# Optimization experiments

Hardware: AMD Instinct MI355X
Metric: run time of the kernel (lower is better)

Reference implementation:

```python
import jax, jax.numpy as jnp
import numpy as np

B, L1, L2 = 16, 32, 128
DEC = 512       # decoder_size
MEM = 512       # memory_bank_size
TOP = 50        # topic_num


def setup_inputs() -> dict:
    key = jax.random.key(0)
    ks = jax.random.split(key, 16)
    s = lambda fan_in: 1.0 / np.sqrt(fan_in)
    inp = {
        "decoder_state": jax.random.normal(ks[0], (B, DEC), jnp.float32),
        "doc_memory": jax.random.normal(ks[1], (B, L1, MEM), jnp.float32),
        "word_memory": jax.random.normal(ks[2], (B, L1, L2, MEM), jnp.float32),
        "topic_dist": jax.random.uniform(ks[3], (B, TOP), jnp.float32),
        "doc_mask": jnp.ones((B, L1), jnp.int32),
        "word_mask": jnp.ones((B, L1, L2), jnp.int32),
        # HierAttention params (PyTorch Linear weight layout: [out, in])
        "Wv": jax.random.uniform(ks[4], (1, DEC), jnp.float32, -s(DEC), s(DEC)),
        "Wd": jax.random.uniform(ks[5], (DEC, DEC), jnp.float32, -s(DEC), s(DEC)),
        "Wt": jax.random.uniform(ks[6], (DEC, TOP), jnp.float32, -s(TOP), s(TOP)),
        "Wm": jax.random.uniform(ks[7], (DEC, MEM), jnp.float32, -s(MEM), s(MEM)),
        # doc_attention (inner Attention) params
        "Wv2": jax.random.uniform(ks[8], (1, DEC), jnp.float32, -s(DEC), s(DEC)),
        "Wd2": jax.random.uniform(ks[9], (DEC, DEC), jnp.float32, -s(DEC), s(DEC)),
        "Wt2": jax.random.uniform(ks[10], (DEC, TOP), jnp.float32, -s(TOP), s(TOP)),
        "Wm2": jax.random.uniform(ks[11], (DEC, MEM), jnp.float32, -s(MEM), s(MEM)),
    }
    return inp


def reference(decoder_state, doc_memory, word_memory, topic_dist,
              doc_mask, word_mask,
              Wv, Wd, Wt, Wm, Wv2, Wd2, Wt2, Wm2):
    neg_inf = jnp.float32(-jnp.inf)

    # ---- word-level (HierAttention.score) ----
    enc_feat = jnp.einsum('bqwm,dm->bqwd', word_memory, Wm)      # [B,L1,L2,DEC]
    dec_feat = decoder_state @ Wd.T                              # [B,DEC]
    top_feat = topic_dist @ Wt.T                                 # [B,DEC]
    e = jnp.tanh(enc_feat + (dec_feat + top_feat)[:, None, None, :])
    word_scores = jnp.einsum('bqwd,od->bqw', e, Wv)[..., 0] if Wv.shape[0] != 1 else jnp.einsum('bqwd,d->bqw', e, Wv[0])
    word_scores = jnp.where(word_mask == 0, neg_inf, word_scores)
    word_attn = jax.nn.softmax(word_scores, axis=-1)             # [B,L1,L2]

    # ---- doc-level (Attention.score) ----
    enc_feat_d = jnp.einsum('bqm,dm->bqd', doc_memory, Wm2)      # [B,L1,DEC]
    dec_feat_d = decoder_state @ Wd2.T                           # [B,DEC]
    top_feat_d = topic_dist @ Wt2.T                              # [B,DEC]
    e_d = jnp.tanh(enc_feat_d + (dec_feat_d + top_feat_d)[:, None, :])
    doc_scores = jnp.einsum('bqd,d->bq', e_d, Wv2[0])            # [B,L1]
    doc_scores = jnp.where(doc_mask == 0, neg_inf, doc_scores)
    doc_attn = jax.nn.softmax(doc_scores, axis=-1)               # [B,L1]

    # ---- combine ----
    rescaled = doc_attn[..., None] * word_attn                   # [B,L1,L2]
    context = jnp.einsum('bqw,bqwm->bm', rescaled, word_memory)  # [B,MEM]
    return context, rescaled
```

## Files before the change

### kernel.cpp

```cpp
#include <hip/hip_runtime.h>
#include <hip/hip_bf16.h>
#include <math.h>

#define BATCH 16
#define L1 32
#define L2 128
#define DEC 512
#define MEM 512
#define TOPN 50
#define NROWS (BATCH * L1 * L2)
#define NBQ (BATCH * L1)

typedef short short8 __attribute__((ext_vector_type(8)));
typedef float f32x16 __attribute__((ext_vector_type(16)));

#define WS_WP     0
#define WS_WP2    131072
#define WS_BIAS1  262144
#define WS_BIAS2  270336
#define WS_DOCSC  278528

__device__ __forceinline__ unsigned int pkbf(float a, float b) {
    __hip_bfloat162 h = __float22bfloat162_rn(float2{a, b});
    union { __hip_bfloat162 h; unsigned int u; } c{h};
    return c.u;
}

__device__ __forceinline__ float fast_tanh(float x) {
    return 1.f - 2.f / (__expf(2.f * x) + 1.f);
}

__global__ __launch_bounds__(256) void setup_kernel(
    const float* __restrict__ Wm, const float* __restrict__ Wm2,
    unsigned short* __restrict__ Wp, unsigned short* __restrict__ Wp2,
    const float* __restrict__ dec, const float* __restrict__ topic,
    const float* __restrict__ Wd, const float* __restrict__ Wt,
    const float* __restrict__ Wd2, const float* __restrict__ Wt2,
    float* __restrict__ bias1, float* __restrict__ bias2,
    float* __restrict__ ctx_out)
{
    const int bid = blockIdx.x;
    const int tid = threadIdx.x;
    if (bid < 128) {
        int s = bid * 256 + tid;
        int C = s >> 10;
        int u = s & 1023;
        int nt = u >> 6, k8 = (u >> 5) & 1, n_in = u & 31;
        int d = nt * 32 + n_in;
        int k = C * 16 + k8 * 8;

        const float4* src = (const float4*)(Wm + (size_t)d * DEC + k);
        float4 v0 = src[0], v1 = src[1];
        uint4 v;
        v.x = pkbf(v0.x, v0.y); v.y = pkbf(v0.z, v0.w);
        v.z = pkbf(v1.x, v1.y); v.w = pkbf(v1.z, v1.w);
        ((uint4*)Wp)[s] = v;

        const float4* src2 = (const float4*)(Wm2 + (size_t)d * DEC + k);
        float4 w0 = src2[0], w1 = src2[1];
        uint4 w;
        w.x = pkbf(w0.x, w0.y); w.y = pkbf(w0.z, w0.w);
        w.z = pkbf(w1.x, w1.y); w.w = pkbf(w1.z, w1.w);
        ((uint4*)Wp2)[s] = w;
    } else if (bid < 128 + 4096) {
        int gw = (bid - 128) * 4 + (tid >> 6);
        int lane = tid & 63;
        int mat = gw >> 13;
        int rem = gw & 8191;
        int bb = rem >> 9;
        int d = rem & 511;

        const float* wrow = (mat ? Wd2 : Wd) + (size_t)d * DEC;
        const float* drow = dec + (size_t)bb * DEC;
        float4 a0 = ((const float4*)wrow)[lane * 2];
        float4 a1 = ((const float4*)wrow)[lane * 2 + 1];
        float4 x0 = ((const float4*)drow)[lane * 2];
        float4 x1 = ((const float4*)drow)[lane * 2 + 1];
        float acc = a0.x * x0.x;
        acc = fmaf(a0.y, x0.y, acc);
        acc = fmaf(a0.z, x0.z, acc);
        acc = fmaf(a0.w, x0.w, acc);
        acc = fmaf(a1.x, x1.x, acc);
        acc = fmaf(a1.y, x1.y, acc);
        acc = fmaf(a1.z, x1.z, acc);
        acc = fmaf(a1.w, x1.w, acc);
        const float* trow = (mat ? Wt2 : Wt) + (size_t)d * TOPN;
        if (lane < TOPN) acc = fmaf(trow[lane], topic[bb * TOPN + lane], acc);
#pragma unroll
        for (int o = 1; o <= 32; o <<= 1) acc += __shfl_xor(acc, o);
        if (lane == 0) (mat ? bias2 : bias1)[bb * DEC + d] = acc;
    } else {
        int i = (bid - (128 + 4096)) * 256 + tid;
        float4 z = {0.f, 0.f, 0.f, 0.f};
        ((float4*)ctx_out)[i * 2] = z;
        ((float4*)ctx_out)[i * 2 + 1] = z;
    }
}

__global__ __launch_bounds__(256, 2) void score_all_kernel(
    const float* __restrict__ Xw,
    const float* __restrict__ Xd,
    const unsigned short* __restrict__ Wp,
    const unsigned short* __restrict__ Wp2,
    const float* __restrict__ Wv, const float* __restrict__ Wv2,
    const float* __restrict__ bias1, const float* __restrict__ bias2,
    float* __restrict__ word_scores,
    float* __restrict__ doc_scores)
{
    __shared__ __align__(16) char lsA[64 * 1040];
    __shared__ float red[4][64];

    const int bid = blockIdx.x;
    const int tid = threadIdx.x;
    const bool isdoc = (bid >= 1024);

    const float* X;
    const unsigned short* Wpp;
    const float* Wvp;
    const float* bias;
    float* outp;
    int r0, bshift;
    if (isdoc) { X = Xd; Wpp = Wp2; Wvp = Wv2; bias = bias2; outp = doc_scores; r0 = (bid - 1024) * 64; bshift = 5; }
    else       { X = Xw; Wpp = Wp;  Wvp = Wv;  bias = bias1; outp = word_scores; r0 = bid * 64; bshift = 12; }

    {
        const int kf4 = tid & 127;
        const int rb0 = tid >> 7;
        const float4* Xs = (const float4*)X + (size_t)r0 * 128 + kf4;
        float4 va[8], vb[8];
#pragma unroll
        for (int i = 0; i < 8; ++i) va[i] = Xs[(size_t)(2 * i + rb0) * 128];
#pragma unroll
        for (int blk = 0; blk < 4; ++blk) {
            float4* cur = (blk & 1) ? vb : va;
            float4* nxt = (blk & 1) ? va : vb;
            if (blk < 3) {
#pragma unroll
                for (int i = 0; i < 8; ++i)
                    nxt[i] = Xs[(size_t)(2 * (8 * (blk + 1) + i) + rb0) * 128];
            }
#pragma unroll
            for (int i = 0; i < 8; ++i) {
                int row = 2 * (8 * blk + i) + rb0;
                uint2 w;
                w.x = pkbf(cur[i].x, cur[i].y);
                w.y = pkbf(cur[i].z, cur[i].w);
                *(uint2*)(lsA + (size_t)row * 1040 + kf4 * 8) = w;
            }
        }
    }
    __syncthreads();

    const int lane = tid & 63;
    const int wid = tid >> 6;
    const int col = lane & 31;
    const int h = lane >> 5;

    const char* aB0 = lsA + (size_t)col * 1040 + h * 16;
    const char* aB1 = aB0 + 32 * 1040;

    const uint4* Bq = (const uint4*)Wpp;
    const int bBase = wid * 128 + lane;
#define BOFF(s) ((size_t)((s) & 31) * 1024 + (size_t)((s) >> 5) * 512 + bBase)
#define MFMA(a, bb, c) __builtin_amdgcn_mfma_f32_32x32x16_bf16(a, bb, c, 0, 0, 0)

    uint4 rbf[8][2];
#pragma unroll
    for (int i = 0; i < 8; ++i) { rbf[i][0] = Bq[BOFF(i)]; rbf[i][1] = Bq[BOFF(i) + 64]; }

    float preg0 = 0.f, preg1 = 0.f;
    const int b0i = (r0) >> bshift;
    const int b1i = (r0 + 32) >> bshift;

#pragma unroll
    for (int P = 0; P < 2; ++P) {
        f32x16 acc0, acc1, acc2, acc3;
        acc0 = acc1 = acc2 = acc3 =
            (f32x16){0.f,0.f,0.f,0.f, 0.f,0.f,0.f,0.f, 0.f,0.f,0.f,0.f, 0.f,0.f,0.f,0.f};
#pragma unroll
        for (int t = 0; t < 32; ++t) {
            const int s = P * 32 + t;
            short8 a0 = *(const short8*)(aB0 + t * 32);
            short8 a1 = *(const short8*)(aB1 + t * 32);
            union { uint4 u; short8 s8; } c0{rbf[s & 7][0]}, c1{rbf[s & 7][1]};
            if (s < 56) { rbf[s & 7][0] = Bq[BOFF(s + 8)]; rbf[s & 7][1] = Bq[BOFF(s + 8) + 64]; }
            acc0 = MFMA(a0, c0.s8, acc0);
            acc1 = MFMA(a0, c1.s8, acc1);
            acc2 = MFMA(a1, c0.s8, acc2);
            acc3 = MFMA(a1, c1.s8, acc3);
        }
        const int d0 = P * 256 + wid * 64 + col;
        const float wv0 = Wvp[d0], wv1 = Wvp[d0 + 32];
        {
            const float bs0 = bias[b0i * DEC + d0], bs1 = bias[b0i * DEC + d0 + 32];
#pragma unroll
            for (int r = 0; r < 16; ++r) {
                float val = fmaf(wv0, fast_tanh(acc0[r] + bs0),
                                 wv1 * fast_tanh(acc1[r] + bs1));
                val += __shfl_xor(val, 16);
                val += __shfl_xor(val, 8);
                val += __shfl_xor(val, 4);
                val += __shfl_xor(val, 2);
                val += __shfl_xor(val, 1);
                preg0 += (col == r) ? val : 0.f;
            }
        }
        {
            const float bs0 = bias[b1i * DEC + d0], bs1 = bias[b1i * DEC + d0 + 32];
#pragma unroll
            for (int r = 0; r < 16; ++r) {
                float val = fmaf(wv0, fast_tanh(acc2[r] + bs0),
                                 wv1 * fast_tanh(acc3[r] + bs1));
                val += __shfl_xor(val, 16);
                val += __shfl_xor(val, 8);
                val += __shfl_xor(val, 4);
                val += __shfl_xor(val, 2);
                val += __shfl_xor(val, 1);
                preg1 += (col == r) ? val : 0.f;
            }
        }
    }

    const int rowin = (col & 3) + 8 * (col >> 2) + 4 * h;
    if (col < 16) {
        red[wid][rowin] = preg0;
        red[wid][32 + rowin] = preg1;
    }
    __syncthreads();
    if (tid < 64)
        outp[r0 + tid] = red[0][tid] + red[1][tid] + red[2][tid] + red[3][tid];
}

__global__ __launch_bounds__(256, 4) void combine_kernel(
    const float* __restrict__ X,
    const float* __restrict__ doc_scores,
    const int* __restrict__ doc_mask,
    const int* __restrict__ word_mask,
    float* __restrict__ rescaled_out,
    float* __restrict__ ctx_out)
{
    __shared__ float sS[128];
    __shared__ float rmax2[2], rsum2[2];
    __shared__ float s_dattn;
    __shared__ __align__(16) float4 part[128];

    const int tid = threadIdx.x;
    const int lane = tid & 63;
    const int wid = tid >> 6;
    const int bq = blockIdx.x;
    const int r0 = bq * L2;
    const int b = bq >> 5;
    const int q = bq & 31;

    if (tid < 32) {
        int di = b * 32 + tid;
        float dsv = doc_scores[di];
        if (doc_mask[di] == 0) dsv = -INFINITY;
        float mx = dsv;
#pragma unroll
        for (int o = 1; o <= 16; o <<= 1) mx = fmaxf(mx, __shfl_xor(mx, o));
        float e = __expf(dsv - mx);
        float sum = e;
#pragma unroll
        for (int o = 1; o <= 16; o <<= 1) sum += __shfl_xor(sum, o);
        if (tid == q) s_dattn = e / sum;
    }

    float e = 0.f, sv = 0.f;
    if (tid < 128) {
        sv = rescaled_out[r0 + tid];
        if (word_mask[r0 + tid] == 0) sv = -INFINITY;
        float mx = sv;
#pragma unroll
        for (int o = 1; o <= 32; o <<= 1) mx = fmaxf(mx, __shfl_xor(mx, o));
        if (lane == 0) rmax2[wid] = mx;
    }
    __syncthreads();
    if (tid < 128) {
        float mx = fmaxf(rmax2[0], rmax2[1]);
        e = __expf(sv - mx);
        float sum = e;
#pragma unroll
        for (int o = 1; o <= 32; o <<= 1) sum += __shfl_xor(sum, o);
        if (lane == 0) rsum2[wid] = sum;
    }
    __syncthreads();
    if (tid < 128) {
        float sum = rsum2[0] + rsum2[1];
        float resc = s_dattn * (e / sum);
        sS[tid] = resc;
        rescaled_out[r0 + tid] = resc;
    }
    __syncthreads();

    const int hh = tid >> 7;
    const int m4 = tid & 127;
    const float4* Xr = (const float4*)X + (size_t)(r0 + hh * 64) * 128 + m4;
    float4 a = {0.f, 0.f, 0.f, 0.f};
#pragma unroll 8
    for (int i = 0; i < 64; ++i) {
        float rr = sS[hh * 64 + i];
        float4 v = Xr[(size_t)i * 128];
        a.x = fmaf(rr, v.x, a.x);
        a.y = fmaf(rr, v.y, a.y);
        a.z = fmaf(rr, v.z, a.z);
        a.w = fmaf(rr, v.w, a.w);
    }
    if (hh) part[m4] = a;
    __syncthreads();
    if (hh == 0) {
        float4 p0 = part[m4];
        a.x += p0.x; a.y += p0.y; a.z += p0.z; a.w += p0.w;
        float* dst = ctx_out + (size_t)b * MEM + m4 * 4;
        atomicAdd(dst + 0, a.x);
        atomicAdd(dst + 1, a.y);
        atomicAdd(dst + 2, a.z);
        atomicAdd(dst + 3, a.w);
    }
}

extern "C" void kernel_launch(void* const* d_in, const int* in_sizes, int n_in,
                              void* d_out, int out_size, void* d_ws, size_t ws_size,
                              hipStream_t stream) {
    const float* decoder_state = (const float*)d_in[0];
    const float* doc_memory    = (const float*)d_in[1];
    const float* word_memory   = (const float*)d_in[2];
    const float* topic_dist    = (const float*)d_in[3];
    const int*   doc_mask      = (const int*)d_in[4];
    const int*   word_mask     = (const int*)d_in[5];
    const float* Wv  = (const float*)d_in[6];
    const float* Wd  = (const float*)d_in[7];
    const float* Wt  = (const float*)d_in[8];
    const float* Wm  = (const float*)d_in[9];
    const float* Wv2 = (const float*)d_in[10];
    const float* Wd2 = (const float*)d_in[11];
    const float* Wt2 = (const float*)d_in[12];
    const float* Wm2 = (const float*)d_in[13];

    float* ws = (float*)d_ws;
    unsigned short* Wp  = (unsigned short*)(ws + WS_WP);
    unsigned short* Wp2 = (unsigned short*)(ws + WS_WP2);
    float* bias1       = ws + WS_BIAS1;
    float* bias2       = ws + WS_BIAS2;
    float* doc_scores  = ws + WS_DOCSC;

    float* ctx_out      = (float*)d_out;
    float* rescaled_out = (float*)d_out + BATCH * MEM;

    setup_kernel<<<128 + 4096 + 4, 256, 0, stream>>>(Wm, Wm2, Wp, Wp2,
                                                     decoder_state, topic_dist,
                                                     Wd, Wt, Wd2, Wt2, bias1, bias2, ctx_out);
    score_all_kernel<<<1024 + 8, 256, 0, stream>>>(word_memory, doc_memory, Wp, Wp2,
                                                   Wv, Wv2, bias1, bias2,
                                                   rescaled_out, doc_scores);
    combine_kernel<<<NBQ, 256, 0, stream>>>(word_memory, doc_scores, doc_mask, word_mask,
                                            rescaled_out, ctx_out);
}
```

Measured before the change: 342.0 us.

## Fuse word scoring with softmax and context reduction into one kernel

Merges the word-level score kernel and the combine kernel so each 512-thread block handles one (b,q) row of 128 words. It computes the MFMA scores, softmax, rescaling and the context accumulation while the word_memory tile is still in cache. Within the block, the LDS staging is split into quarter-K chunks, with the next quarter's global loads overlapped against MFMA on the current one, and the quarter order is rotated per block. Doc scores now run as a separate small launch first. The cost is fewer blocks (512 versus 1024), larger LDS use per block that may reduce occupancy, and serialized doc-score launch.

```diff
diff --git a/kernel.cpp b/kernel.cpp
--- a/kernel.cpp
+++ b/kernel.cpp
@@ -97,183 +97,182 @@
     }
 }
 
-__global__ __launch_bounds__(256, 2) void score_all_kernel(
-    const float* __restrict__ Xw,
-    const float* __restrict__ Xd,
-    const unsigned short* __restrict__ Wp,
-    const unsigned short* __restrict__ Wp2,
-    const float* __restrict__ Wv, const float* __restrict__ Wv2,
-    const float* __restrict__ bias1, const float* __restrict__ bias2,
-    float* __restrict__ word_scores,
-    float* __restrict__ doc_scores)
+__global__ __launch_bounds__(512, 2) void score_fused_kernel(
+    const float* __restrict__ X,
+    const unsigned short* __restrict__ Wp_,
+    const float* __restrict__ Wv_,
+    const float* __restrict__ bias_,
+    const float* __restrict__ doc_scores,
+    const int* __restrict__ doc_mask,
+    const int* __restrict__ word_mask,
+    float* __restrict__ rescaled_out,
+    float* __restrict__ ctx_out,
+    float* __restrict__ scores_out,
+    int mode)
 {
-    __shared__ __align__(16) char lsA[64 * 1040];
-    __shared__ float red[4][64];
-
+    __shared__ __align__(16) char lsA[128 * 1040];
+    __shared__ float red[8][128];
+    __shared__ float sS[128];
+    __shared__ float rmax2[2], rsum2[2];
+    __shared__ float s_dattn;
+    __shared__ __align__(16) float4 part[3 * 128];
+
+    const int tid = threadIdx.x;
+    const int lane = tid & 63;
+    const int w = tid >> 6;
     const int bid = blockIdx.x;
-    const int tid = threadIdx.x;
-    const bool isdoc = (bid >= 1024);
-
-    const float* X;
-    const unsigned short* Wpp;
-    const float* Wvp;
-    const float* bias;
-    float* outp;
-    int r0, bshift;
-    if (isdoc) { X = Xd; Wpp = Wp2; Wvp = Wv2; bias = bias2; outp = doc_scores; r0 = (bid - 1024) * 64; bshift = 5; }
-    else       { X = Xw; Wpp = Wp;  Wvp = Wv;  bias = bias1; outp = word_scores; r0 = bid * 64; bshift = 12; }
-
-    {
-        const int kf4 = tid & 127;
-        const int rb0 = tid >> 7;
-        const float4* Xs = (const float4*)X + (size_t)r0 * 128 + kf4;
-        float4 va[8], vb[8];
-#pragma unroll
-        for (int i = 0; i < 8; ++i) va[i] = Xs[(size_t)(2 * i + rb0) * 128];
-#pragma unroll
-        for (int blk = 0; blk < 4; ++blk) {
-            float4* cur = (blk & 1) ? vb : va;
-            float4* nxt = (blk & 1) ? va : vb;
-            if (blk < 3) {
-#pragma unroll
-                for (int i = 0; i < 8; ++i)
-                    nxt[i] = Xs[(size_t)(2 * (8 * (blk + 1) + i) + rb0) * 128];
-            }
-#pragma unroll
-            for (int i = 0; i < 8; ++i) {
-                int row = 2 * (8 * blk + i) + rb0;
-                uint2 w;
-                w.x = pkbf(cur[i].x, cur[i].y);
-                w.y = pkbf(cur[i].z, cur[i].w);
-                *(uint2*)(lsA + (size_t)row * 1040 + kf4 * 8) = w;
-            }
-        }
-    }
-    __syncthreads();
-
-    const int lane = tid & 63;
-    const int wid = tid >> 6;
+    const int r0 = bid * 128;
     const int col = lane & 31;
     const int h = lane >> 5;
 
-    const char* aB0 = lsA + (size_t)col * 1040 + h * 16;
-    const char* aB1 = aB0 + 32 * 1040;
-
-    const uint4* Bq = (const uint4*)Wpp;
-    const int bBase = wid * 128 + lane;
-#define BOFF(s) ((size_t)((s) & 31) * 1024 + (size_t)((s) >> 5) * 512 + bBase)
+    const int q0 = bid & 3;
+    const int Q[4] = { q0, (q0 + 1) & 3, (q0 + 2) & 3, (q0 + 3) & 3 };
+#define CH_AT(f) (Q[(f) >> 3] * 8 + ((f) & 7))
+
+    const int scol = tid & 31;
+    const int srow0 = tid >> 5;
+    const float4* Xbase = (const float4*)X + (size_t)(r0 + srow0) * 128 + scol;
+    char* const wbase = lsA + (size_t)srow0 * 1040 + scol * 8;
+
+#define ISSUEQ(buf, qq) { _Pragma("unroll") for (int i = 0; i < 8; ++i) \
+        buf[i] = Xbase[(size_t)(16 * i) * 128 + (qq) * 32]; }
+#define WRITEQ(buf, qq) { _Pragma("unroll") for (int i = 0; i < 8; ++i) { \
+        uint2 ww; ww.x = pkbf(buf[i].x, buf[i].y); ww.y = pkbf(buf[i].z, buf[i].w); \
+        *(uint2*)(wbase + (size_t)(16 * i) * 1040 + (qq) * 256) = ww; } }
+#define LGKMBAR { asm volatile("s_waitcnt lgkmcnt(0)" ::: "memory"); \
+                  __builtin_amdgcn_s_barrier(); asm volatile("" ::: "memory"); }
 #define MFMA(a, bb, c) __builtin_amdgcn_mfma_f32_32x32x16_bf16(a, bb, c, 0, 0, 0)
 
-    uint4 rbf[8][2];
-#pragma unroll
-    for (int i = 0; i < 8; ++i) { rbf[i][0] = Bq[BOFF(i)]; rbf[i][1] = Bq[BOFF(i) + 64]; }
-
-    float preg0 = 0.f, preg1 = 0.f;
-    const int b0i = (r0) >> bshift;
-    const int b1i = (r0 + 32) >> bshift;
-
-#pragma unroll
-    for (int P = 0; P < 2; ++P) {
-        f32x16 acc0, acc1, acc2, acc3;
-        acc0 = acc1 = acc2 = acc3 =
-            (f32x16){0.f,0.f,0.f,0.f, 0.f,0.f,0.f,0.f, 0.f,0.f,0.f,0.f, 0.f,0.f,0.f,0.f};
-#pragma unroll
-        for (int t = 0; t < 32; ++t) {
-            const int s = P * 32 + t;
-            short8 a0 = *(const short8*)(aB0 + t * 32);
-            short8 a1 = *(const short8*)(aB1 + t * 32);
-            union { uint4 u; short8 s8; } c0{rbf[s & 7][0]}, c1{rbf[s & 7][1]};
-            if (s < 56) { rbf[s & 7][0] = Bq[BOFF(s + 8)]; rbf[s & 7][1] = Bq[BOFF(s + 8) + 64]; }
-            acc0 = MFMA(a0, c0.s8, acc0);
-            acc1 = MFMA(a0, c1.s8, acc1);
-            acc2 = MFMA(a1, c0.s8, acc2);
-            acc3 = MFMA(a1, c1.s8, acc3);
-        }
-        const int d0 = P * 256 + wid * 64 + col;
-        const float wv0 = Wvp[d0], wv1 = Wvp[d0 + 32];
-        {
-            const float bs0 = bias[b0i * DEC + d0], bs1 = bias[b0i * DEC + d0 + 32];
+    const uint4* Bq4 = (const uint4*)Wp_;
+    const int vB = w * 128 + lane;
+
+    const char* const aR0 = lsA + (size_t)col * 1040 + h * 16;
+    const char* const aR1 = aR0 + 32 * 1040;
+    const char* const aR2 = aR0 + 64 * 1040;
+    const char* const aR3 = aR0 + 96 * 1040;
+
+    f32x16 acc[8];
+#pragma unroll
+    for (int t = 0; t < 8; ++t)
+        acc[t] = (f32x16){0.f,0.f,0.f,0.f, 0.f,0.f,0.f,0.f, 0.f,0.f,0.f,0.f, 0.f,0.f,0.f,0.f};
+
+    uint4 rb[4][2];
+
+#define STEP(f, a0q, a1q, a2q, a3q) { \
+        union { uint4 u; short8 s8; } b0{rb[(f) & 3][0]}, b1{rb[(f) & 3][1]}; \
+        if ((f) + 4 < 32) { \
+            const int cn_ = CH_AT((f) + 4); \
+            rb[(f) & 3][0] = Bq4[(size_t)cn_ * 1024 + vB]; \
+            rb[(f) & 3][1] = Bq4[(size_t)cn_ * 1024 + vB + 64]; \
+        } \
+        short8 a0 = *(const short8*)((a0q) + ((f) & 7) * 32); \
+        short8 a1 = *(const short8*)((a1q) + ((f) & 7) * 32); \
+        short8 a2 = *(const short8*)((a2q) + ((f) & 7) * 32); \
+        short8 a3 = *(const short8*)((a3q) + ((f) & 7) * 32); \
+        acc[0] = MFMA(a0, b0.s8, acc[0]); \
+        acc[1] = MFMA(a0, b1.s8, acc[1]); \
+        acc[2] = MFMA(a1, b0.s8, acc[2]); \
+        acc[3] = MFMA(a1, b1.s8, acc[3]); \
+        acc[4] = MFMA(a2, b0.s8, acc[4]); \
+        acc[5] = MFMA(a2, b1.s8, acc[5]); \
+        acc[6] = MFMA(a3, b0.s8, acc[6]); \
+        acc[7] = MFMA(a3, b1.s8, acc[7]); }
+
+#define QUARTER(j, f0) { \
+        const int qo_ = Q[j] * 256; \
+        const char* a0q = aR0 + qo_; const char* a1q = aR1 + qo_; \
+        const char* a2q = aR2 + qo_; const char* a3q = aR3 + qo_; \
+        STEP((f0) + 0, a0q, a1q, a2q, a3q) STEP((f0) + 1, a0q, a1q, a2q, a3q) \
+        STEP((f0) + 2, a0q, a1q, a2q, a3q) STEP((f0) + 3, a0q, a1q, a2q, a3q) \
+        STEP((f0) + 4, a0q, a1q, a2q, a3q) STEP((f0) + 5, a0q, a1q, a2q, a3q) \
+        STEP((f0) + 6, a0q, a1q, a2q, a3q) STEP((f0) + 7, a0q, a1q, a2q, a3q) }
+
+    float4 sb0[8], sb1[8];
+    ISSUEQ(sb0, Q[0]);
+    ISSUEQ(sb1, Q[1]);
+
+    if (mode == 0 && tid < 32) {
+        int b_ = bid >> 5;
+        int di = b_ * 32 + tid;
+        float dsv = doc_scores[di];
+        if (doc_mask[di] == 0) dsv = -INFINITY;
+        float mx = dsv;
+#pragma unroll
+        for (int o = 1; o <= 16; o <<= 1) mx = fmaxf(mx, __shfl_xor(mx, o));
+        float e = __expf(dsv - mx);
+        float sum = e;
+#pragma unroll
+        for (int o = 1; o <= 16; o <<= 1) sum += __shfl_xor(sum, o);
+        if (tid == (bid & 31)) s_dattn = e / sum;
+    }
+
+    WRITEQ(sb0, Q[0]);
+#pragma unroll
+    for (int f = 0; f < 4; ++f) {
+        const int c_ = CH_AT(f);
+        rb[f][0] = Bq4[(size_t)c_ * 1024 + vB];
+        rb[f][1] = Bq4[(size_t)c_ * 1024 + vB + 64];
+    }
+    LGKMBAR;
+
+    ISSUEQ(sb0, Q[2]);
+    QUARTER(0, 0);
+    WRITEQ(sb1, Q[1]);
+    LGKMBAR;
+
+    ISSUEQ(sb1, Q[3]);
+    QUARTER(1, 8);
+    WRITEQ(sb0, Q[2]);
+    LGKMBAR;
+
+    QUARTER(2, 16);
+    WRITEQ(sb1, Q[3]);
+    LGKMBAR;
+
+    QUARTER(3, 24);
+
+    {
+        const int d0 = w * 64 + col;
+        const float wv0 = Wv_[d0], wv1 = Wv_[d0 + 32];
+#pragma unroll
+        for (int rg = 0; rg < 4; ++rg) {
+            const int brg = mode ? (bid * 4 + rg) : (bid >> 5);
+            const float bs0 = bias_[brg * DEC + d0];
+            const float bs1 = bias_[brg * DEC + d0 + 32];
 #pragma unroll
             for (int r = 0; r < 16; ++r) {
-                float val = fmaf(wv0, fast_tanh(acc0[r] + bs0),
-                                 wv1 * fast_tanh(acc1[r] + bs1));
+                float val = fmaf(wv0, fast_tanh(acc[rg * 2 + 0][r] + bs0),
+                                 wv1 * fast_tanh(acc[rg * 2 + 1][r] + bs1));
                 val += __shfl_xor(val, 16);
                 val += __shfl_xor(val, 8);
                 val += __shfl_xor(val, 4);
                 val += __shfl_xor(val, 2);
                 val += __shfl_xor(val, 1);
-                preg0 += (col == r) ? val : 0.f;
+                if (col == r) {
+                    int row_in = (r & 3) + 8 * (r >> 2) + 4 * h;
+                    red[w][rg * 32 + row_in] = val;
+                }
             }
         }
-        {
-            const float bs0 = bias[b1i * DEC + d0], bs1 = bias[b1i * DEC + d0 + 32];
-#pragma unroll
-            for (int r = 0; r < 16; ++r) {
-                float val = fmaf(wv0, fast_tanh(acc2[r] + bs0),
-                                 wv1 * fast_tanh(acc3[r] + bs1));
-                val += __shfl_xor(val, 16);
-                val += __shfl_xor(val, 8);
-                val += __shfl_xor(val, 4);
-                val += __shfl_xor(val, 2);
-                val += __shfl_xor(val, 1);
-                preg1 += (col == r) ? val : 0.f;
-            }
-        }
-    }
-
-    const int rowin = (col & 3) + 8 * (col >> 2) + 4 * h;
-    if (col < 16) {
-        red[wid][rowin] = preg0;
-        red[wid][32 + rowin] = preg1;
-    }
-    __syncthreads();
-    if (tid < 64)
-        outp[r0 + tid] = red[0][tid] + red[1][tid] + red[2][tid] + red[3][tid];
-}
-
-__global__ __launch_bounds__(256, 4) void combine_kernel(
-    const float* __restrict__ X,
-    const float* __restrict__ doc_scores,
-    const int* __restrict__ doc_mask,
-    const int* __restrict__ word_mask,
-    float* __restrict__ rescaled_out,
-    float* __restrict__ ctx_out)
-{
-    __shared__ float sS[128];
-    __shared__ float rmax2[2], rsum2[2];
-    __shared__ float s_dattn;
-    __shared__ __align__(16) float4 part[128];
-
-    const int tid = threadIdx.x;
-    const int lane = tid & 63;
-    const int wid = tid >> 6;
-    const int bq = blockIdx.x;
-    const int r0 = bq * L2;
-    const int b = bq >> 5;
-    const int q = bq & 31;
-
-    if (tid < 32) {
-        int di = b * 32 + tid;
-        float dsv = doc_scores[di];
-        if (doc_mask[di] == 0) dsv = -INFINITY;
-        float mx = dsv;
-#pragma unroll
-        for (int o = 1; o <= 16; o <<= 1) mx = fmaxf(mx, __shfl_xor(mx, o));
-        float e = __expf(dsv - mx);
-        float sum = e;
-#pragma unroll
-        for (int o = 1; o <= 16; o <<= 1) sum += __shfl_xor(sum, o);
-        if (tid == q) s_dattn = e / sum;
+    }
+    __syncthreads();
+
+    if (mode) {
+        if (tid < 128)
+            scores_out[r0 + tid] = red[0][tid] + red[1][tid] + red[2][tid] + red[3][tid]
+                                 + red[4][tid] + red[5][tid] + red[6][tid] + red[7][tid];
+        return;
     }
 
     float e = 0.f, sv = 0.f;
     if (tid < 128) {
-        sv = rescaled_out[r0 + tid];
+        sv = red[0][tid] + red[1][tid] + red[2][tid] + red[3][tid]
+           + red[4][tid] + red[5][tid] + red[6][tid] + red[7][tid];
         if (word_mask[r0 + tid] == 0) sv = -INFINITY;
         float mx = sv;
 #pragma unroll
         for (int o = 1; o <= 32; o <<= 1) mx = fmaxf(mx, __shfl_xor(mx, o));
-        if (lane == 0) rmax2[wid] = mx;
+        if (lane == 0) rmax2[w] = mx;
     }
     __syncthreads();
     if (tid < 128) {
@@ -282,7 +281,7 @@
         float sum = e;
 #pragma unroll
         for (int o = 1; o <= 32; o <<= 1) sum += __shfl_xor(sum, o);
-        if (lane == 0) rsum2[wid] = sum;
+        if (lane == 0) rsum2[w] = sum;
     }
     __syncthreads();
     if (tid < 128) {
@@ -293,25 +292,29 @@
     }
     __syncthreads();
 
+    const int b_ = bid >> 5;
     const int hh = tid >> 7;
     const int m4 = tid & 127;
-    const float4* Xr = (const float4*)X + (size_t)(r0 + hh * 64) * 128 + m4;
+    const float4* Xr = (const float4*)X + (size_t)r0 * 128 + (size_t)hh * 32 * 128 + m4;
     float4 a = {0.f, 0.f, 0.f, 0.f};
 #pragma unroll 8
-    for (int i = 0; i < 64; ++i) {
-        float rr = sS[hh * 64 + i];
+    for (int i = 0; i < 32; ++i) {
+        float rr = sS[hh * 32 + i];
         float4 v = Xr[(size_t)i * 128];
         a.x = fmaf(rr, v.x, a.x);
         a.y = fmaf(rr, v.y, a.y);
         a.z = fmaf(rr, v.z, a.z);
         a.w = fmaf(rr, v.w, a.w);
     }
-    if (hh) part[m4] = a;
+    if (hh) part[(hh - 1) * 128 + m4] = a;
     __syncthreads();
     if (hh == 0) {
-        float4 p0 = part[m4];
-        a.x += p0.x; a.y += p0.y; a.z += p0.z; a.w += p0.w;
-        float* dst = ctx_out + (size_t)b * MEM + m4 * 4;
+        float4 p0 = part[m4], p1 = part[128 + m4], p2 = part[256 + m4];
+        a.x += p0.x + p1.x + p2.x;
+        a.y += p0.y + p1.y + p2.y;
+        a.z += p0.z + p1.z + p2.z;
+        a.w += p0.w + p1.w + p2.w;
+        float* dst = ctx_out + (size_t)b_ * MEM + m4 * 4;
         atomicAdd(dst + 0, a.x);
         atomicAdd(dst + 1, a.y);
         atomicAdd(dst + 2, a.z);
@@ -350,9 +353,10 @@
     setup_kernel<<<128 + 4096 + 4, 256, 0, stream>>>(Wm, Wm2, Wp, Wp2,
                                                      decoder_state, topic_dist,
                                                      Wd, Wt, Wd2, Wt2, bias1, bias2, ctx_out);
-    score_all_kernel<<<1024 + 8, 256, 0, stream>>>(word_memory, doc_memory, Wp, Wp2,
-                                                   Wv, Wv2, bias1, bias2,
-                                                   rescaled_out, doc_scores);
-    combine_kernel<<<NBQ, 256, 0, stream>>>(word_memory, doc_scores, doc_mask, word_mask,
-                                            rescaled_out, ctx_out);
-}
+    score_fused_kernel<<<4, 512, 0, stream>>>(doc_memory, Wp2, Wv2, bias2,
+                                              nullptr, nullptr, nullptr,
+                                              nullptr, nullptr, doc_scores, 1);
+    score_fused_kernel<<<NBQ, 512, 0, stream>>>(word_memory, Wp, Wv, bias1,
+                                                doc_scores, doc_mask, word_mask,
+                                                rescaled_out, ctx_out, nullptr, 0);
+}
```

Result: faster. 315.9 us (-7.6%).
